# Kernel optimization log

Hardware: AMD Instinct MI355X
Metric: run time of the kernel (lower is better)

The kernel has to match this reference:

```python
import jax, jax.numpy as jnp
import numpy as np

NUM_CAPSULE = 32
DIM_VECTOR = 16
NUM_ROUTING = 3

def squash(v, axis=-1):
    s2 = jnp.sum(jnp.square(v), axis=axis, keepdims=True)
    scale = s2 / (1.0 + s2) / jnp.sqrt(s2)
    return scale * v

def setup_inputs() -> dict:
    key = jax.random.key(0)
    k1, k2 = jax.random.split(key)
    B, IN_CAPS, IN_DIM = 64, 2048, 8
    x = jax.random.normal(k1, (B, IN_CAPS, IN_DIM), dtype=jnp.float32)
    # glorot-uniform-ish weight: [in_caps, num_caps, in_dim, out_dim]
    limit = np.sqrt(6.0 / (IN_DIM + DIM_VECTOR)).astype(np.float32)
    W = jax.random.uniform(k2, (IN_CAPS, NUM_CAPSULE, IN_DIM, DIM_VECTOR), dtype=jnp.float32, minval=-limit, maxval=limit)
    return {"x": x, "W": W}

def reference(x, W):
    # x: [B, in_caps, in_dim]; W: [in_caps, num_caps, in_dim, out_dim]
    # inputs_hat (u_hat): [B, in_caps, num_caps, out_dim]
    u_hat = jnp.einsum('bid,inde->bine', x, W)
    B, IN_CAPS = u_hat.shape[0], u_hat.shape[1]
    # routing logits; original broadcasts over out_dim with identical values,
    # so a trailing singleton dim is mathematically equivalent
    b = jnp.zeros((B, IN_CAPS, NUM_CAPSULE, 1), dtype=u_hat.dtype)
    v = None
    for i in range(NUM_ROUTING):
        c = jax.nn.softmax(b, axis=2)                       # over num_capsule
        s = jnp.sum(c * u_hat, axis=1, keepdims=True)       # [B,1,nc,out]
        v = squash(s)                                       # [B,1,nc,out]
        if i != NUM_ROUTING - 1:
            b = b + jnp.sum(u_hat * v, axis=-1, keepdims=True)
    return v.reshape(-1, NUM_CAPSULE, DIM_VECTOR)
```

## Files before the change

### kernel.cpp

```cpp
#include <hip/hip_runtime.h>
#include <math.h>


#define B_TOT 64
#define I_TOT 2048
#define D_IN  8
#define NC    32
#define EV    16
#define OD    (NC*EV)
#define BC    8
#define NBC   (B_TOT/BC)
#define ICH   16
#define NIC   (I_TOT/ICH)

__device__ __forceinline__ void fma4(float4& acc, float a, const float4& w) {
    acc.x = fmaf(a, w.x, acc.x);
    acc.y = fmaf(a, w.y, acc.y);
    acc.z = fmaf(a, w.z, acc.z);
    acc.w = fmaf(a, w.w, acc.w);
}

template <int MODE>
__global__ __launch_bounds__(256, 4)
void route_pass(const float* __restrict__ x, const float* __restrict__ W,
                float* __restrict__ P, const float* __restrict__ vin,
                float* __restrict__ aws)
{
    __shared__ __align__(16) float xl[BC * ICH * D_IN];
    __shared__ float wsum[2][4][BC];

    const int t  = threadIdx.x;
    const int ic = blockIdx.x & (NIC - 1);
    const int bc = blockIdx.x >> 7;
    const int b0 = bc * BC;
    const int i0 = ic * ICH;
    const int eq = t & 3;
    const int bh = (t >> 2) & 1;
    const int n  = t >> 3;
    const int w  = t >> 6;

    {
        const int row = t >> 5, f = (t & 31) * 4;
        *(float4*)&xl[row * (ICH * D_IN) + f] =
            *(const float4*)&x[((size_t)(b0 + row) * I_TOT + i0) * D_IN + f];
    }

    float4 vr[4];
    if (MODE >= 1) {
        #pragma unroll
        for (int q = 0; q < 4; ++q)
            vr[q] = *(const float4*)&vin[(size_t)(b0 + bh * 4 + q) * OD + n * EV + eq * 4];
    }
    __syncthreads();

    float4 sacc[4];
    #pragma unroll
    for (int q = 0; q < 4; ++q) sacc[q] = make_float4(0.f, 0.f, 0.f, 0.f);

    const float* Wt = &W[(size_t)i0 * 4096 + n * 128 + eq * 4];

    for (int ii = 0; ii < ICH; ++ii) {
        float4 wr[8];
        #pragma unroll
        for (int d = 0; d < 8; ++d)
            wr[d] = *(const float4*)&Wt[ii * 4096 + d * 16];

        float4 u[4];
        #pragma unroll
        for (int q = 0; q < 4; ++q) {
            const int bl = bh * 4 + q;
            float4 xa = *(float4*)&xl[bl * (ICH * D_IN) + ii * 8];
            float4 xb = *(float4*)&xl[bl * (ICH * D_IN) + ii * 8 + 4];
            float4 uu = make_float4(0.f, 0.f, 0.f, 0.f);
            fma4(uu, xa.x, wr[0]); fma4(uu, xa.y, wr[1]);
            fma4(uu, xa.z, wr[2]); fma4(uu, xa.w, wr[3]);
            fma4(uu, xb.x, wr[4]); fma4(uu, xb.y, wr[5]);
            fma4(uu, xb.z, wr[6]); fma4(uu, xb.w, wr[7]);
            u[q] = uu;
        }

        if (MODE == 0) {
            #pragma unroll
            for (int q = 0; q < 4; ++q) {
                sacc[q].x += u[q].x; sacc[q].y += u[q].y;
                sacc[q].z += u[q].z; sacc[q].w += u[q].w;
            }
        } else {
            float a[4];
            #pragma unroll
            for (int q = 0; q < 4; ++q) {
                float ap = u[q].x * vr[q].x + u[q].y * vr[q].y
                         + u[q].z * vr[q].z + u[q].w * vr[q].w;
                ap += __shfl_xor(ap, 1, 64);
                ap += __shfl_xor(ap, 2, 64);
                a[q] = ap;
            }
            const size_t aoff = (((size_t)(i0 + ii) * NBC + bc) * NC + n) * 8 + bh * 4;
            if (MODE == 2) {
                float4 a0 = *(const float4*)&aws[aoff];
                a[0] += a0.x; a[1] += a0.y; a[2] += a0.z; a[3] += a0.w;
            }
            if (MODE == 1 && eq == 0) {
                float4 st = make_float4(a[0], a[1], a[2], a[3]);
                *(float4*)&aws[aoff] = st;
            }
            float e[4], p[4];
            #pragma unroll
            for (int q = 0; q < 4; ++q) {
                e[q] = __expf(a[q]);
                float pp = e[q];
                pp += __shfl_xor(pp, 8, 64);
                pp += __shfl_xor(pp, 16, 64);
                pp += __shfl_xor(pp, 32, 64);
                p[q] = pp;
            }
            if (eq == 0) {
                #pragma unroll
                for (int q = 0; q < 4; ++q)
                    wsum[ii & 1][w][bh * 4 + q] = p[q];
            }
            __syncthreads();
            #pragma unroll
            for (int q = 0; q < 4; ++q) {
                const int bl = bh * 4 + q;
                float s = wsum[ii & 1][0][bl] + wsum[ii & 1][1][bl]
                        + wsum[ii & 1][2][bl] + wsum[ii & 1][3][bl];
                float c = e[q] / s;
                fma4(sacc[q], c, u[q]);
            }
        }
    }

    #pragma unroll
    for (int q = 0; q < 4; ++q)
        *(float4*)&P[((size_t)ic * B_TOT + b0 + bh * 4 + q) * OD + n * EV + eq * 4] = sacc[q];
}

__global__ __launch_bounds__(256, 4)
void reduce_squash(const float* __restrict__ P, float* __restrict__ dst, float pre)
{
    const int b = blockIdx.x;
    const int t = threadIdx.x;
    float s1 = 0.f, s2 = 0.f;
    for (int ic = 0; ic < NIC; ++ic) {
        const float* p = &P[((size_t)ic * B_TOT + b) * OD];
        s1 += p[t];
        s2 += p[t + 256];
    }
    s1 *= pre; s2 *= pre;
    float q1 = s1 * s1, q2 = s2 * s2;
    q1 += __shfl_xor(q1, 1, 64);  q2 += __shfl_xor(q2, 1, 64);
    q1 += __shfl_xor(q1, 2, 64);  q2 += __shfl_xor(q2, 2, 64);
    q1 += __shfl_xor(q1, 4, 64);  q2 += __shfl_xor(q2, 4, 64);
    q1 += __shfl_xor(q1, 8, 64);  q2 += __shfl_xor(q2, 8, 64);
    float sc1 = q1 / ((1.0f + q1) * sqrtf(q1));
    float sc2 = q2 / ((1.0f + q2) * sqrtf(q2));
    dst[b * OD + t]       = s1 * sc1;
    dst[b * OD + t + 256] = s2 * sc2;
}

extern "C" void kernel_launch(void* const* d_in, const int* in_sizes, int n_in,
                              void* d_out, int out_size, void* d_ws, size_t ws_size,
                              hipStream_t stream) {
    const float* x = (const float*)d_in[0];
    const float* W = (const float*)d_in[1];
    float* out = (float*)d_out;

    char* ws = (char*)d_ws;
    float* P   = (float*)ws;
    float* aws = (float*)(ws + (size_t)16 * 1024 * 1024);
    float* v0  = (float*)(ws + (size_t)32 * 1024 * 1024);
    float* v1  = v0 + B_TOT * OD;

    dim3 grid(NBC * NIC), blk(256);

    route_pass<0><<<grid, blk, 0, stream>>>(x, W, P, nullptr, nullptr);
    reduce_squash<<<B_TOT, 256, 0, stream>>>(P, v0, 1.0f / 32.0f);
    route_pass<1><<<grid, blk, 0, stream>>>(x, W, P, v0, aws);
    reduce_squash<<<B_TOT, 256, 0, stream>>>(P, v1, 1.0f);
    route_pass<2><<<grid, blk, 0, stream>>>(x, W, P, v1, aws);
    reduce_squash<<<B_TOT, 256, 0, stream>>>(P, out, 1.0f);
}
```

Before: 198.7 us.

## Fold routing logits into summed v, prefetch W, widen reduce_squash grid

```diff
diff --git a/kernel.cpp b/kernel.cpp
--- a/kernel.cpp
+++ b/kernel.cpp
@@ -4,12 +4,10 @@
 
 #define B_TOT 64
 #define I_TOT 2048
-#define D_IN  8
 #define NC    32
 #define EV    16
 #define OD    (NC*EV)
 #define BC    8
-#define NBC   (B_TOT/BC)
 #define ICH   16
 #define NIC   (I_TOT/ICH)
 
@@ -23,10 +21,9 @@
 template <int MODE>
 __global__ __launch_bounds__(256, 4)
 void route_pass(const float* __restrict__ x, const float* __restrict__ W,
-                float* __restrict__ P, const float* __restrict__ vin,
-                float* __restrict__ aws)
+                float* __restrict__ P, const float* __restrict__ vin)
 {
-    __shared__ __align__(16) float xl[BC * ICH * D_IN];
+    __shared__ __align__(16) float xl[BC * ICH * 8];
     __shared__ float wsum[2][4][BC];
 
     const int t  = threadIdx.x;
@@ -40,13 +37,13 @@
     const int w  = t >> 6;
 
     {
-        const int row = t >> 5, f = (t & 31) * 4;
-        *(float4*)&xl[row * (ICH * D_IN) + f] =
-            *(const float4*)&x[((size_t)(b0 + row) * I_TOT + i0) * D_IN + f];
+        const int f = t * 4, row = t >> 5, off = f & 127;
+        *(float4*)&xl[row * 128 + off] =
+            *(const float4*)&x[((size_t)(b0 + row) * I_TOT + i0) * 8 + off];
     }
 
     float4 vr[4];
-    if (MODE >= 1) {
+    if (MODE == 1) {
         #pragma unroll
         for (int q = 0; q < 4; ++q)
             vr[q] = *(const float4*)&vin[(size_t)(b0 + bh * 4 + q) * OD + n * EV + eq * 4];
@@ -57,57 +54,59 @@
     #pragma unroll
     for (int q = 0; q < 4; ++q) sacc[q] = make_float4(0.f, 0.f, 0.f, 0.f);
 
-    const float* Wt = &W[(size_t)i0 * 4096 + n * 128 + eq * 4];
+    const float* Wb = W + (size_t)i0 * 4096 + n * 128 + eq * 4;
 
+    float4 wreg[2][8];
+    #pragma unroll
+    for (int d = 0; d < 8; ++d)
+        wreg[0][d] = *(const float4*)&Wb[d * 16];
+
+    #pragma unroll
     for (int ii = 0; ii < ICH; ++ii) {
-        float4 wr[8];
-        #pragma unroll
-        for (int d = 0; d < 8; ++d)
-            wr[d] = *(const float4*)&Wt[ii * 4096 + d * 16];
-
-        float4 u[4];
-        #pragma unroll
-        for (int q = 0; q < 4; ++q) {
-            const int bl = bh * 4 + q;
-            float4 xa = *(float4*)&xl[bl * (ICH * D_IN) + ii * 8];
-            float4 xb = *(float4*)&xl[bl * (ICH * D_IN) + ii * 8 + 4];
-            float4 uu = make_float4(0.f, 0.f, 0.f, 0.f);
-            fma4(uu, xa.x, wr[0]); fma4(uu, xa.y, wr[1]);
-            fma4(uu, xa.z, wr[2]); fma4(uu, xa.w, wr[3]);
-            fma4(uu, xb.x, wr[4]); fma4(uu, xb.y, wr[5]);
-            fma4(uu, xb.z, wr[6]); fma4(uu, xb.w, wr[7]);
-            u[q] = uu;
+        const int cur = ii & 1, nxt = cur ^ 1;
+        if (ii + 1 < ICH) {
+            #pragma unroll
+            for (int d = 0; d < 8; ++d)
+                wreg[nxt][d] = *(const float4*)&Wb[(ii + 1) * 4096 + d * 16];
         }
 
         if (MODE == 0) {
             #pragma unroll
             for (int q = 0; q < 4; ++q) {
-                sacc[q].x += u[q].x; sacc[q].y += u[q].y;
-                sacc[q].z += u[q].z; sacc[q].w += u[q].w;
+                const int bl = bh * 4 + q;
+                float4 xa = *(float4*)&xl[bl * 128 + ii * 8];
+                float4 xb = *(float4*)&xl[bl * 128 + ii * 8 + 4];
+                fma4(sacc[q], xa.x, wreg[cur][0]); fma4(sacc[q], xa.y, wreg[cur][1]);
+                fma4(sacc[q], xa.z, wreg[cur][2]); fma4(sacc[q], xa.w, wreg[cur][3]);
+                fma4(sacc[q], xb.x, wreg[cur][4]); fma4(sacc[q], xb.y, wreg[cur][5]);
+                fma4(sacc[q], xb.z, wreg[cur][6]); fma4(sacc[q], xb.w, wreg[cur][7]);
             }
         } else {
-            float a[4];
+            float4 u[4];
+            #pragma unroll
+            for (int q = 0; q < 4; ++q) {
+                const int bl = bh * 4 + q;
+                float4 xa = *(float4*)&xl[bl * 128 + ii * 8];
+                float4 xb = *(float4*)&xl[bl * 128 + ii * 8 + 4];
+                float4 uu = make_float4(0.f, 0.f, 0.f, 0.f);
+                fma4(uu, xa.x, wreg[cur][0]); fma4(uu, xa.y, wreg[cur][1]);
+                fma4(uu, xa.z, wreg[cur][2]); fma4(uu, xa.w, wreg[cur][3]);
+                fma4(uu, xb.x, wreg[cur][4]); fma4(uu, xb.y, wreg[cur][5]);
+                fma4(uu, xb.z, wreg[cur][6]); fma4(uu, xb.w, wreg[cur][7]);
+                u[q] = uu;
+            }
+            float e[4];
             #pragma unroll
             for (int q = 0; q < 4; ++q) {
                 float ap = u[q].x * vr[q].x + u[q].y * vr[q].y
                          + u[q].z * vr[q].z + u[q].w * vr[q].w;
                 ap += __shfl_xor(ap, 1, 64);
                 ap += __shfl_xor(ap, 2, 64);
-                a[q] = ap;
+                e[q] = __expf(ap);
             }
-            const size_t aoff = (((size_t)(i0 + ii) * NBC + bc) * NC + n) * 8 + bh * 4;
-            if (MODE == 2) {
-                float4 a0 = *(const float4*)&aws[aoff];
-                a[0] += a0.x; a[1] += a0.y; a[2] += a0.z; a[3] += a0.w;
-            }
-            if (MODE == 1 && eq == 0) {
-                float4 st = make_float4(a[0], a[1], a[2], a[3]);
-                *(float4*)&aws[aoff] = st;
-            }
-            float e[4], p[4];
+            float p[4];
             #pragma unroll
             for (int q = 0; q < 4; ++q) {
-                e[q] = __expf(a[q]);
                 float pp = e[q];
                 pp += __shfl_xor(pp, 8, 64);
                 pp += __shfl_xor(pp, 16, 64);
@@ -117,16 +116,15 @@
             if (eq == 0) {
                 #pragma unroll
                 for (int q = 0; q < 4; ++q)
-                    wsum[ii & 1][w][bh * 4 + q] = p[q];
+                    wsum[cur][w][bh * 4 + q] = p[q];
             }
             __syncthreads();
             #pragma unroll
             for (int q = 0; q < 4; ++q) {
                 const int bl = bh * 4 + q;
-                float s = wsum[ii & 1][0][bl] + wsum[ii & 1][1][bl]
-                        + wsum[ii & 1][2][bl] + wsum[ii & 1][3][bl];
-                float c = e[q] / s;
-                fma4(sacc[q], c, u[q]);
+                float s = wsum[cur][0][bl] + wsum[cur][1][bl]
+                        + wsum[cur][2][bl] + wsum[cur][3][bl];
+                fma4(sacc[q], e[q] / s, u[q]);
             }
         }
     }
@@ -136,27 +134,34 @@
         *(float4*)&P[((size_t)ic * B_TOT + b0 + bh * 4 + q) * OD + n * EV + eq * 4] = sacc[q];
 }
 
-__global__ __launch_bounds__(256, 4)
-void reduce_squash(const float* __restrict__ P, float* __restrict__ dst, float pre)
+__global__ __launch_bounds__(64)
+void reduce_squash(const float* __restrict__ P, float* __restrict__ dst,
+                   float pre, const float* __restrict__ addv)
 {
-    const int b = blockIdx.x;
-    const int t = threadIdx.x;
-    float s1 = 0.f, s2 = 0.f;
-    for (int ic = 0; ic < NIC; ++ic) {
-        const float* p = &P[((size_t)ic * B_TOT + b) * OD];
-        s1 += p[t];
-        s2 += p[t + 256];
+    const int b = blockIdx.x >> 3, og = blockIdx.x & 7, t = threadIdx.x;
+    const int o = og * 64 + t;
+    float s0 = 0.f, s1 = 0.f, s2 = 0.f, s3 = 0.f;
+    float s4 = 0.f, s5 = 0.f, s6 = 0.f, s7 = 0.f;
+    for (int ic = 0; ic < NIC; ic += 8) {
+        s0 += P[((size_t)(ic + 0) * B_TOT + b) * OD + o];
+        s1 += P[((size_t)(ic + 1) * B_TOT + b) * OD + o];
+        s2 += P[((size_t)(ic + 2) * B_TOT + b) * OD + o];
+        s3 += P[((size_t)(ic + 3) * B_TOT + b) * OD + o];
+        s4 += P[((size_t)(ic + 4) * B_TOT + b) * OD + o];
+        s5 += P[((size_t)(ic + 5) * B_TOT + b) * OD + o];
+        s6 += P[((size_t)(ic + 6) * B_TOT + b) * OD + o];
+        s7 += P[((size_t)(ic + 7) * B_TOT + b) * OD + o];
     }
-    s1 *= pre; s2 *= pre;
-    float q1 = s1 * s1, q2 = s2 * s2;
-    q1 += __shfl_xor(q1, 1, 64);  q2 += __shfl_xor(q2, 1, 64);
-    q1 += __shfl_xor(q1, 2, 64);  q2 += __shfl_xor(q2, 2, 64);
-    q1 += __shfl_xor(q1, 4, 64);  q2 += __shfl_xor(q2, 4, 64);
-    q1 += __shfl_xor(q1, 8, 64);  q2 += __shfl_xor(q2, 8, 64);
-    float sc1 = q1 / ((1.0f + q1) * sqrtf(q1));
-    float sc2 = q2 / ((1.0f + q2) * sqrtf(q2));
-    dst[b * OD + t]       = s1 * sc1;
-    dst[b * OD + t + 256] = s2 * sc2;
+    float s = (((s0 + s1) + (s2 + s3)) + ((s4 + s5) + (s6 + s7))) * pre;
+    float q = s * s;
+    q += __shfl_xor(q, 1, 64);
+    q += __shfl_xor(q, 2, 64);
+    q += __shfl_xor(q, 4, 64);
+    q += __shfl_xor(q, 8, 64);
+    float sc = q / ((1.0f + q) * sqrtf(q));
+    float r = s * sc;
+    if (addv) r += addv[(size_t)b * OD + o];
+    dst[(size_t)b * OD + o] = r;
 }
 
 extern "C" void kernel_launch(void* const* d_in, const int* in_sizes, int n_in,
@@ -167,17 +172,16 @@
     float* out = (float*)d_out;
 
     char* ws = (char*)d_ws;
-    float* P   = (float*)ws;
-    float* aws = (float*)(ws + (size_t)16 * 1024 * 1024);
-    float* v0  = (float*)(ws + (size_t)32 * 1024 * 1024);
-    float* v1  = v0 + B_TOT * OD;
+    float* P    = (float*)ws;
+    float* v0   = (float*)(ws + (size_t)16 * 1024 * 1024);
+    float* vsum = v0 + B_TOT * OD;
 
-    dim3 grid(NBC * NIC), blk(256);
+    dim3 grid(8 * NIC), blk(256);
 
-    route_pass<0><<<grid, blk, 0, stream>>>(x, W, P, nullptr, nullptr);
-    reduce_squash<<<B_TOT, 256, 0, stream>>>(P, v0, 1.0f / 32.0f);
-    route_pass<1><<<grid, blk, 0, stream>>>(x, W, P, v0, aws);
-    reduce_squash<<<B_TOT, 256, 0, stream>>>(P, v1, 1.0f);
-    route_pass<2><<<grid, blk, 0, stream>>>(x, W, P, v1, aws);
-    reduce_squash<<<B_TOT, 256, 0, stream>>>(P, out, 1.0f);
+    route_pass<0><<<grid, blk, 0, stream>>>(x, W, P, nullptr);
+    reduce_squash<<<B_TOT * 8, 64, 0, stream>>>(P, v0, 1.0f / 32.0f, nullptr);
+    route_pass<1><<<grid, blk, 0, stream>>>(x, W, P, v0);
+    reduce_squash<<<B_TOT * 8, 64, 0, stream>>>(P, vsum, 1.0f, v0);
+    route_pass<1><<<grid, blk, 0, stream>>>(x, W, P, vsum);
+    reduce_squash<<<B_TOT * 8, 64, 0, stream>>>(P, out, 1.0f, nullptr);
 }
```

After: 720.1 us. 3.62x slower.
